# Kernel optimization log

Hardware: AMD Instinct MI355X
Metric: run time of the kernel (lower is better)

The kernel has to match this reference:

```python
import jax, jax.numpy as jnp
import numpy as np

INIT_SCALE = 5

def _steps(n_full):
    half = [i + 1 for i in range(0, int(n_full) + 1, 2)]
    return list(reversed(half[1:])) + half

STEP_H = np.array(_steps(192 / INIT_SCALE), dtype=np.float32)  # len 39
STEP_W = np.array(_steps(256 / INIT_SCALE), dtype=np.float32)  # len 51
MASK_H, MASK_W = len(STEP_H), len(STEP_W)


def _prelu(x, a):
    return jnp.maximum(x, 0.0) + a * jnp.minimum(x, 0.0)


def _reduce(x, w, b, a):
    # Conv2dBlock(64,4,1,1,norm='none',activation='prelu'): activation BEFORE 1x1 conv (per source)
    return jnp.einsum('nchw,oc->nohw', _prelu(x, a), w) + b[None, :, None, None]


def _crop_coords(cx, cy, H, W):
    # replicates floor(center - mask/2) / floor(center + mask/2) + border clamping
    top = cy - (MASK_H + 1) // 2
    bottom = cy + MASK_H // 2
    left = cx - (MASK_W + 1) // 2
    right = cx + MASK_W // 2
    dy1 = jnp.maximum(-top, 0)
    dy2 = jnp.maximum(bottom - H, 0)
    dx1 = jnp.maximum(-left, 0)
    dx2 = jnp.maximum(right - W, 0)
    new_top = top + dy1
    new_left = left + dx1
    new_h = jnp.maximum(bottom - dy2 - new_top, 0)
    new_w = jnp.maximum(right - dx2 - new_left, 0)
    return new_top, new_left, new_h, new_w, dy1, dx1


def _gimg(img, rows, cols):  # img (C,H,W) -> (C,len(rows),len(cols))
    return img[:, rows[:, None], cols[None, :]]


def _gmask(m, rows, cols):  # m (MASK_H,MASK_W)
    return m[rows[:, None], cols[None, :]]


def _forward(location, fea_c, fea_p, scale_param, H, W, c_landmark, p_landmark, w1, b1, a1, w2, b2, a2):
    N = fea_c.shape[0]
    ratio = H // fea_c.shape[2]
    fea_cn = _reduce(jnp.repeat(jnp.repeat(fea_c, ratio, 2), ratio, 3), w1, b1, a1)
    fea_pn = _reduce(jnp.repeat(jnp.repeat(fea_p, ratio, 2), ratio, 3), w2, b2, a2)
    C = fea_cn.shape[1]

    init_h = W / INIT_SCALE  # note: swapped vs H/W, exactly as in the original forward
    init_w = H / INIT_SCALE
    sig = jax.nn.sigmoid
    adj_cw, adj_ch = scale_param[:, :, 0, 0], scale_param[:, :, 0, 1]
    adj_pw, adj_ph = scale_param[:, :, 1, 0], scale_param[:, :, 1, 1]
    step_h = jnp.asarray(STEP_H)
    step_w = jnp.asarray(STEP_W)

    def box_mask(adj_h, adj_w):
        h = (init_h * sig(adj_h))[..., None]  # (N,32,1)
        w = (init_w * sig(adj_w))[..., None]
        return sig((h - step_h) * 2)[..., :, None] * sig((w - step_w) * 2)[..., None, :]

    src_mask = box_mask(adj_ch, adj_cw)  # (N,32,39,51)
    tar_mask = box_mask(adj_ph, adj_pw)

    r_ar = jnp.arange(MASK_H, dtype=jnp.int32)
    c_ar = jnp.arange(MASK_W, dtype=jnp.int32)
    c_cx, c_cy = c_landmark[:, :, 0], c_landmark[:, :, 1]
    p_cx, p_cy = p_landmark[:, :, 0], p_landmark[:, :, 1]
    use_lm = ~(((c_cx == 0) & (c_cy == 0)) | ((p_cx == 0) & (p_cy == 0)))  # (N,32)

    def make_patch(fea, lm_mask, cx, cy):
        top, left, nh, nw, dy1, dx1 = _crop_coords(cx, cy, H, W)
        rows = jnp.clip(top[..., None] + r_ar, 0, H - 1)        # (N,32,39)
        cols = jnp.clip(left[..., None] + c_ar, 0, W - 1)       # (N,32,51)
        mrows = jnp.clip(dy1[..., None] + r_ar, 0, MASK_H - 1)
        mcols = jnp.clip(dx1[..., None] + c_ar, 0, MASK_W - 1)
        valid = (use_lm[..., None, None]
                 & (r_ar[None, None, :, None] < nh[..., None, None])
                 & (c_ar[None, None, None, :] < nw[..., None, None]))  # (N,32,39,51)
        g = jax.vmap(lambda f, R, Cc: jax.vmap(_gimg, in_axes=(None, 0, 0))(f, R, Cc))(fea, rows, cols)  # (N,32,C,39,51)
        m = jax.vmap(jax.vmap(_gmask))(lm_mask, mrows, mcols)  # (N,32,39,51)
        patch = jnp.where(valid[:, :, None], g * m[:, :, None], 0.0)
        return patch, rows, cols, valid

    cloth, rows_c, cols_c, valid_c = make_patch(fea_cn, src_mask, c_cx, c_cy)
    person, rows_p, cols_p, valid_p = make_patch(fea_pn, tar_mask, p_cx, p_cy)

    loc5 = location.reshape(N, 32, 2, H, W)
    loc_g = jax.vmap(jax.vmap(_gimg))(loc5, rows_c, cols_c)  # (N,32,2,39,51)
    loc_patch = jnp.where(valid_c[:, :, None], loc_g, -1.0)  # -1 fill as in source

    L = MASK_H * MASK_W
    P = person.reshape(N, 32, C, L)
    K = cloth.reshape(N, 32, C, L)
    V = loc_patch.reshape(N, 32, 2, L)
    scores = jnp.einsum('nicp,nicq->nipq', P, K)  # (N,32,L,L) query=person px, key=cloth px
    corr = jax.nn.softmax(scores, axis=-1)
    flow_patch = jnp.einsum('nipq,nidq->nidp', corr, V).reshape(N, 32, 2, MASK_H, MASK_W)

    # scatter person-crop regions back into full-res outputs (invalid -> dump row/col H,W)
    rr = jnp.where(valid_p, jnp.broadcast_to(rows_p[:, :, :, None], valid_p.shape), H)
    cc = jnp.where(valid_p, jnp.broadcast_to(cols_p[:, :, None, :], valid_p.shape), W)
    bb = jnp.arange(N)[:, None, None, None]
    ii = jnp.arange(32)[None, :, None, None]
    flow_pad = jnp.full((N, 32, H + 1, W + 1, 2), -1.0, dtype=flow_patch.dtype)
    flow_pad = flow_pad.at[bb, ii, rr, cc].set(flow_patch.transpose(0, 1, 3, 4, 2))
    landmark_flow = flow_pad[:, :, :H, :W, :].transpose(0, 1, 4, 2, 3).reshape(N, 64, H, W)
    mask = jnp.zeros((N, 32, H + 1, W + 1), dtype=flow_patch.dtype).at[bb, ii, rr, cc].set(1.0)[:, :, :H, :W]
    return landmark_flow, mask


def setup_inputs() -> dict:
    key = jax.random.key(0)
    ks = jax.random.split(key, 8)
    N, H, W = 1, 192, 256
    fh, fw = H // 4, W // 4
    return {
        'location': jax.random.normal(ks[0], (N, 64, H, W), jnp.float32),
        'fea_c': jax.random.normal(ks[1], (N, 64, fh, fw), jnp.float32),
        'fea_p': jax.random.normal(ks[2], (N, 64, fh, fw), jnp.float32),
        'scale_param': jax.random.normal(ks[3], (N, 32, 2, 2), jnp.float32),
        'H': H,
        'W': W,
        'c_landmark': jax.random.randint(ks[4], (N, 32, 2), 0, 180, jnp.int32),
        'p_landmark': jax.random.randint(ks[5], (N, 32, 2), 0, 180, jnp.int32),
        'w1': jax.random.normal(ks[6], (4, 64), jnp.float32) * 0.05,
        'b1': jnp.zeros((4,), jnp.float32),
        'a1': jnp.array(0.25, jnp.float32),
        'w2': jax.random.normal(ks[7], (4, 64), jnp.float32) * 0.05,
        'b2': jnp.zeros((4,), jnp.float32),
        'a2': jnp.array(0.25, jnp.float32),
    }


def reference(location, fea_c, fea_p, scale_param, H, W, c_landmark, p_landmark, w1, b1, a1, w2, b2, a2):
    return _forward(location, fea_c, fea_p, scale_param, H, W, c_landmark, p_landmark, w1, b1, a1, w2, b2, a2)
```

## Files before the change

kernel.cpp:

```cpp
#include <hip/hip_runtime.h>

constexpr int kH = 192, kW = 256, kHW = kH * kW;
constexpr int kFH = 48, kFW = 64, kFHW = kFH * kFW;
constexpr int kMH = 39, kMW = 51;
constexpr int kL = kMH * kMW;
constexpr int kLP = 2048;
constexpr int kHeads = 32;
constexpr float kInitH = 256.0f / 5.0f;
constexpr float kInitW = 192.0f / 5.0f;
constexpr float kL2E = 1.44269504088896340736f;
constexpr float kBias = -16.0f;
constexpr float kPadCorr = 59.0f / 65536.0f;

typedef float v2f __attribute__((ext_vector_type(2)));
__device__ __forceinline__ v2f pkfma(v2f a, v2f b, v2f c) {
  return __builtin_elementwise_fma(a, b, c);
}

__device__ __forceinline__ float fast_exp2(float x) {
#if __has_builtin(__builtin_amdgcn_exp2f)
  return __builtin_amdgcn_exp2f(x);
#else
  float r;
  asm("v_exp_f32 %0, %1\n\ts_nop 1" : "=v"(r) : "v"(x));
  return r;
#endif
}

struct HeadParams {
  int use;
  int ntop_c, nleft_c, nh_c, nw_c, dy1_c, dx1_c;
  int ntop_p, nleft_p, nh_p, nw_p, dy1_p, dx1_p;
  float h_c, w_c, h_p, w_p;
};

__device__ __forceinline__ float sigf(float x) { return 1.0f / (1.0f + __expf(-x)); }
__device__ __forceinline__ float stepH(int j) { return (float)(2 * abs(j - 19) + 1); }
__device__ __forceinline__ float stepW(int j) { return (float)(2 * abs(j - 25) + 1); }

__device__ void headParams(int i, const int* clm, const int* plm, const float* sp, HeadParams& h) {
  int ccx = clm[2 * i], ccy = clm[2 * i + 1];
  int pcx = plm[2 * i], pcy = plm[2 * i + 1];
  h.use = !(((ccx == 0) && (ccy == 0)) || ((pcx == 0) && (pcy == 0)));
  {
    int top = ccy - (kMH + 1) / 2, bottom = ccy + kMH / 2;
    int left = ccx - (kMW + 1) / 2, right = ccx + kMW / 2;
    int dy1 = max(-top, 0), dy2 = max(bottom - kH, 0);
    int dx1 = max(-left, 0), dx2 = max(right - kW, 0);
    h.ntop_c = top + dy1; h.nleft_c = left + dx1; h.dy1_c = dy1; h.dx1_c = dx1;
    h.nh_c = max(kMH - dy1 - dy2, 0); h.nw_c = max(kMW - dx1 - dx2, 0);
  }
  {
    int top = pcy - (kMH + 1) / 2, bottom = pcy + kMH / 2;
    int left = pcx - (kMW + 1) / 2, right = pcx + kMW / 2;
    int dy1 = max(-top, 0), dy2 = max(bottom - kH, 0);
    int dx1 = max(-left, 0), dx2 = max(right - kW, 0);
    h.ntop_p = top + dy1; h.nleft_p = left + dx1; h.dy1_p = dy1; h.dx1_p = dx1;
    h.nh_p = max(kMH - dy1 - dy2, 0); h.nw_p = max(kMW - dx1 - dx2, 0);
  }
  float adj_cw = sp[4 * i + 0], adj_ch = sp[4 * i + 1];
  float adj_pw = sp[4 * i + 2], adj_ph = sp[4 * i + 3];
  h.h_c = kInitH * sigf(adj_ch);
  h.w_c = kInitW * sigf(adj_cw);
  h.h_p = kInitH * sigf(adj_ph);
  h.w_p = kInitW * sigf(adj_pw);
}

__global__ void k_init(float4* __restrict__ out, int n4, int nflow4) {
  int i = blockIdx.x * 256 + threadIdx.x;
  if (i < n4) {
    float v = (i < nflow4) ? -1.0f : 0.0f;
    out[i] = make_float4(v, v, v, v);
  }
}

__global__ void k_reduce(const float* __restrict__ fc, const float* __restrict__ fp,
                         const float* __restrict__ w1, const float* __restrict__ b1, const float* __restrict__ a1,
                         const float* __restrict__ w2, const float* __restrict__ b2, const float* __restrict__ a2,
                         float* __restrict__ fr) {
  int gid = blockIdx.x * 256 + threadIdx.x;
  if (gid >= 2 * kFHW) return;
  int which = gid / kFHW;
  int pix = gid - which * kFHW;
  const float* f = which ? fp : fc;
  const float* w = which ? w2 : w1;
  const float* b = which ? b2 : b1;
  float a = which ? a2[0] : a1[0];
  float acc0 = 0.f, acc1 = 0.f, acc2 = 0.f, acc3 = 0.f;
  for (int c = 0; c < 64; ++c) {
    float x = f[c * kFHW + pix];
    float pr = fmaxf(x, 0.f) + a * fminf(x, 0.f);
    acc0 = fmaf(pr, w[c], acc0);
    acc1 = fmaf(pr, w[64 + c], acc1);
    acc2 = fmaf(pr, w[128 + c], acc2);
    acc3 = fmaf(pr, w[192 + c], acc3);
  }
  float* o = fr + which * 4 * kFHW;
  o[pix]            = acc0 + b[0];
  o[kFHW + pix]     = acc1 + b[1];
  o[2 * kFHW + pix] = acc2 + b[2];
  o[3 * kFHW + pix] = acc3 + b[3];
}

__global__ void k_patch(const float* __restrict__ fr, const float* __restrict__ loc,
                        const float* __restrict__ sp, const int* __restrict__ clm, const int* __restrict__ plm,
                        float* __restrict__ Kpl, float* __restrict__ Vpl, float4* __restrict__ Pall) {
  int i = blockIdx.y;
  int q = blockIdx.x * 256 + threadIdx.x;
  HeadParams hp; headParams(i, clm, plm, sp, hp);
  int qr = q / kMW, qc = q - qr * kMW;
  constexpr int PS = kHeads * kLP;
  int o = i * kLP + q;
  {
    bool val = (q < kL) && hp.use && (qr < hp.nh_c) && (qc < hp.nw_c);
    int row = min(hp.ntop_c + qr, kH - 1);
    int col = min(hp.nleft_c + qc, kW - 1);
    int mr = min(hp.dy1_c + qr, kMH - 1);
    int mc = min(hp.dx1_c + qc, kMW - 1);
    float mv = sigf((hp.h_c - stepH(mr)) * 2.f) * sigf((hp.w_c - stepW(mc)) * 2.f);
    int fpix = (row >> 2) * kFW + (col >> 2);
    float kx = 0.f, ky = 0.f, kz = 0.f, kw = 0.f, vx = -1.f, vy = -1.f;
    if (val) {
      kx = fr[fpix] * mv;
      ky = fr[kFHW + fpix] * mv;
      kz = fr[2 * kFHW + fpix] * mv;
      kw = fr[3 * kFHW + fpix] * mv;
      vx = loc[(2 * i) * kHW + row * kW + col];
      vy = loc[(2 * i + 1) * kHW + row * kW + col];
    }
    Kpl[o] = kx; Kpl[PS + o] = ky; Kpl[2 * PS + o] = kz; Kpl[3 * PS + o] = kw;
    Vpl[o] = vx; Vpl[PS + o] = vy;
  }
  if (q < kL) {
    bool val = hp.use && (qr < hp.nh_p) && (qc < hp.nw_p);
    int row = min(hp.ntop_p + qr, kH - 1);
    int col = min(hp.nleft_p + qc, kW - 1);
    int mr = min(hp.dy1_p + qr, kMH - 1);
    int mc = min(hp.dx1_p + qc, kMW - 1);
    float mv = sigf((hp.h_p - stepH(mr)) * 2.f) * sigf((hp.w_p - stepW(mc)) * 2.f) * kL2E;
    int fpix = (row >> 2) * kFW + (col >> 2);
    float4 pv = make_float4(0.f, 0.f, 0.f, 0.f);
    if (val) {
      const float* frp = fr + 4 * kFHW;
      pv.x = frp[fpix] * mv;
      pv.y = frp[kFHW + fpix] * mv;
      pv.z = frp[2 * kFHW + fpix] * mv;
      pv.w = frp[3 * kFHW + fpix] * mv;
    }
    Pall[i * kL + q] = pv;
  }
}

template<int QLEN>
__global__ void __launch_bounds__(256) k_attn_t(const float* __restrict__ Kpl, const float* __restrict__ Vpl,
                                                const float4* __restrict__ Pall,
                                                float* __restrict__ pD, float* __restrict__ pX,
                                                float* __restrict__ pY) {
  constexpr int PS = kHeads * kLP;
  int i = blockIdx.z;
  int qsi = blockIdx.y;
  int p = blockIdx.x * 249 + threadIdx.x;
  int pe = min(p, kL - 1);
  const int base = i * kLP + qsi * QLEN;
  const float* kx = Kpl + base;
  const float* ky = Kpl + PS + base;
  const float* kz = Kpl + 2 * PS + base;
  const float* kw = Kpl + 3 * PS + base;
  const float* vx = Vpl + base;
  const float* vy = Vpl + PS + base;
  float4 P = Pall[i * kL + pe];
  v2f PX = {P.x, P.x}, PY = {P.y, P.y}, PZ = {P.z, P.z}, PW = {P.w, P.w};
  const v2f B = {kBias, kBias};
  v2f dA = {0.f, 0.f}, dB = {0.f, 0.f};
  v2f xA = {0.f, 0.f}, xB = {0.f, 0.f};
  v2f yA = {0.f, 0.f}, yB = {0.f, 0.f};
#pragma unroll 8
  for (int t = 0; t < QLEN; t += 4) {
    v2f sA = pkfma(PW, *(const v2f*)(kw + t), B);
    sA = pkfma(PZ, *(const v2f*)(kz + t), sA);
    sA = pkfma(PY, *(const v2f*)(ky + t), sA);
    sA = pkfma(PX, *(const v2f*)(kx + t), sA);
    v2f sB = pkfma(PW, *(const v2f*)(kw + t + 2), B);
    sB = pkfma(PZ, *(const v2f*)(kz + t + 2), sB);
    sB = pkfma(PY, *(const v2f*)(ky + t + 2), sB);
    sB = pkfma(PX, *(const v2f*)(kx + t + 2), sB);
    v2f eA = {fast_exp2(sA.x), fast_exp2(sA.y)};
    v2f eB = {fast_exp2(sB.x), fast_exp2(sB.y)};
    dA += eA;
    xA = pkfma(eA, *(const v2f*)(vx + t), xA);
    yA = pkfma(eA, *(const v2f*)(vy + t), yA);
    dB += eB;
    xB = pkfma(eB, *(const v2f*)(vx + t + 2), xB);
    yB = pkfma(eB, *(const v2f*)(vy + t + 2), yB);
  }
  int o = (i * gridDim.y + qsi) * kLP + pe;
  pD[o] = dA.x + dA.y + dB.x + dB.y;
  pX[o] = xA.x + xA.y + xB.x + xB.y;
  pY[o] = yA.x + yA.y + yB.x + yB.y;
}

__global__ void k_merge(const float* __restrict__ pD, const float* __restrict__ pX, const float* __restrict__ pY,
                        int QS,
                        const float* __restrict__ sp, const int* __restrict__ clm, const int* __restrict__ plm,
                        float* __restrict__ out) {
  int i = blockIdx.y;
  int p = blockIdx.x * 256 + threadIdx.x;
  if (p >= kL) return;
  HeadParams hp; headParams(i, clm, plm, sp, hp);

  int pr = p / kMW, pc = p - pr * kMW;
  bool val = hp.use && (pr < hp.nh_p) && (pc < hp.nw_p);
  if (!val) return;

  float den = -kPadCorr, n0 = kPadCorr, n1 = kPadCorr;
  for (int k = 0; k < QS; ++k) {
    int o = (i * QS + k) * kLP + p;
    den += pD[o]; n0 += pX[o]; n1 += pY[o];
  }
  float inv = 1.0f / den;
  float f0 = n0 * inv, f1 = n1 * inv;

  int R = hp.ntop_p + pr;
  int C = hp.nleft_p + pc;
  out[(2 * i) * kHW + R * kW + C] = f0;
  out[(2 * i + 1) * kHW + R * kW + C] = f1;
  out[64 * kHW + i * kHW + R * kW + C] = 1.0f;
}

extern "C" void kernel_launch(void* const* d_in, const int* in_sizes, int n_in,
                              void* d_out, int out_size, void* d_ws, size_t ws_size,
                              hipStream_t stream) {
  (void)in_sizes; (void)n_in;
  const float* loc = (const float*)d_in[0];
  const float* fc  = (const float*)d_in[1];
  const float* fp  = (const float*)d_in[2];
  const float* sp  = (const float*)d_in[3];
  const int* clm   = (const int*)d_in[6];
  const int* plm   = (const int*)d_in[7];
  const float* w1  = (const float*)d_in[8];
  const float* b1  = (const float*)d_in[9];
  const float* a1  = (const float*)d_in[10];
  const float* w2  = (const float*)d_in[11];
  const float* b2  = (const float*)d_in[12];
  const float* a2  = (const float*)d_in[13];
  float* out = (float*)d_out;
  char* ws = (char*)d_ws;

  float*  fr   = (float*)(ws);
  float*  Kpl  = (float*)(ws + 98304);
  float*  Vpl  = (float*)(ws + 1146880);
  float4* Pall = (float4*)(ws + 1671168);
  size_t base = 2689536;
  size_t perQS = (size_t)3 * kHeads * kLP * 4;
  int QS = 1;
  if (ws_size >= base + 16 * perQS) QS = 16;
  else if (ws_size >= base + 8 * perQS) QS = 8;
  else if (ws_size >= base + 4 * perQS) QS = 4;
  else if (ws_size >= base + 2 * perQS) QS = 2;
  float* pD = (float*)(ws + base);
  float* pX = pD + (size_t)QS * kHeads * kLP;
  float* pY = pX + (size_t)QS * kHeads * kLP;

  int n4 = out_size / 4;
  int nflow4 = 64 * kHW / 4;
  k_init<<<(n4 + 255) / 256, 256, 0, stream>>>((float4*)out, n4, nflow4);
  k_reduce<<<(2 * kFHW + 255) / 256, 256, 0, stream>>>(fc, fp, w1, b1, a1, w2, b2, a2, fr);
  k_patch<<<dim3(kLP / 256, kHeads), 256, 0, stream>>>(fr, loc, sp, clm, plm, Kpl, Vpl, Pall);
  dim3 ag(8, QS, kHeads);
  switch (QS) {
    case 16: k_attn_t<128><<<ag, 256, 0, stream>>>(Kpl, Vpl, Pall, pD, pX, pY); break;
    case 8:  k_attn_t<256><<<ag, 256, 0, stream>>>(Kpl, Vpl, Pall, pD, pX, pY); break;
    case 4:  k_attn_t<512><<<ag, 256, 0, stream>>>(Kpl, Vpl, Pall, pD, pX, pY); break;
    case 2:  k_attn_t<1024><<<ag, 256, 0, stream>>>(Kpl, Vpl, Pall, pD, pX, pY); break;
    default: k_attn_t<2048><<<ag, 256, 0, stream>>>(Kpl, Vpl, Pall, pD, pX, pY); break;
  }
  k_merge<<<dim3((kL + 255) / 256, kHeads), 256, 0, stream>>>(pD, pX, pY, QS, sp, clm, plm, out);
}
```

Baseline: 59.83 us.

## Fuse output init into full-image merge and precompute per-head parameters

Removes the separate k_init kernel by having the merge kernel cover every output pixel, writing either the computed flow and mask or the default fill values. Per-head crop parameters are computed once by an extra block in the reduce kernel, stored in workspace and read by patch and merge instead of being recomputed per thread. This drops one launch and avoids a double write of the output, at the cost of merge launching far more threads (full image per head) and a heavier extra block in the pre kernel.

```diff
diff --git a/kernel.cpp b/kernel.cpp
--- a/kernel.cpp
+++ b/kernel.cpp
@@ -66,20 +66,26 @@
   h.w_p = kInitW * sigf(adj_pw);
 }
 
-__global__ void k_init(float4* __restrict__ out, int n4, int nflow4) {
-  int i = blockIdx.x * 256 + threadIdx.x;
-  if (i < n4) {
-    float v = (i < nflow4) ? -1.0f : 0.0f;
-    out[i] = make_float4(v, v, v, v);
-  }
-}
-
-__global__ void k_reduce(const float* __restrict__ fc, const float* __restrict__ fp,
-                         const float* __restrict__ w1, const float* __restrict__ b1, const float* __restrict__ a1,
-                         const float* __restrict__ w2, const float* __restrict__ b2, const float* __restrict__ a2,
-                         float* __restrict__ fr) {
-  int gid = blockIdx.x * 256 + threadIdx.x;
-  if (gid >= 2 * kFHW) return;
+__global__ void k_pre(const float* __restrict__ fc, const float* __restrict__ fp,
+                      const float* __restrict__ w1, const float* __restrict__ b1, const float* __restrict__ a1,
+                      const float* __restrict__ w2, const float* __restrict__ b2, const float* __restrict__ a2,
+                      const float* __restrict__ sp, const int* __restrict__ clm, const int* __restrict__ plm,
+                      float* __restrict__ fr, int* __restrict__ hpws) {
+  int bx = blockIdx.x;
+  if (bx == 24) {
+    int i = threadIdx.x;
+    if (i < kHeads) {
+      HeadParams h; headParams(i, clm, plm, sp, h);
+      int* o = hpws + i * 20;
+      o[0] = h.use;
+      o[1] = h.ntop_c; o[2] = h.nleft_c; o[3] = h.nh_c; o[4] = h.nw_c; o[5] = h.dy1_c; o[6] = h.dx1_c;
+      o[7] = h.ntop_p; o[8] = h.nleft_p; o[9] = h.nh_p; o[10] = h.nw_p; o[11] = h.dy1_p; o[12] = h.dx1_p;
+      o[13] = __float_as_int(h.h_c); o[14] = __float_as_int(h.w_c);
+      o[15] = __float_as_int(h.h_p); o[16] = __float_as_int(h.w_p);
+    }
+    return;
+  }
+  int gid = bx * 256 + threadIdx.x;
   int which = gid / kFHW;
   int pix = gid - which * kFHW;
   const float* f = which ? fp : fc;
@@ -103,21 +109,26 @@
 }
 
 __global__ void k_patch(const float* __restrict__ fr, const float* __restrict__ loc,
-                        const float* __restrict__ sp, const int* __restrict__ clm, const int* __restrict__ plm,
+                        const int* __restrict__ hpws,
                         float* __restrict__ Kpl, float* __restrict__ Vpl, float4* __restrict__ Pall) {
   int i = blockIdx.y;
   int q = blockIdx.x * 256 + threadIdx.x;
-  HeadParams hp; headParams(i, clm, plm, sp, hp);
+  const int* hp = hpws + i * 20;
+  int use = hp[0];
+  int ntop_c = hp[1], nleft_c = hp[2], nh_c = hp[3], nw_c = hp[4], dy1_c = hp[5], dx1_c = hp[6];
+  int ntop_p = hp[7], nleft_p = hp[8], nh_p = hp[9], nw_p = hp[10], dy1_p = hp[11], dx1_p = hp[12];
+  float h_c = __int_as_float(hp[13]), w_c = __int_as_float(hp[14]);
+  float h_p = __int_as_float(hp[15]), w_p = __int_as_float(hp[16]);
   int qr = q / kMW, qc = q - qr * kMW;
   constexpr int PS = kHeads * kLP;
   int o = i * kLP + q;
   {
-    bool val = (q < kL) && hp.use && (qr < hp.nh_c) && (qc < hp.nw_c);
-    int row = min(hp.ntop_c + qr, kH - 1);
-    int col = min(hp.nleft_c + qc, kW - 1);
-    int mr = min(hp.dy1_c + qr, kMH - 1);
-    int mc = min(hp.dx1_c + qc, kMW - 1);
-    float mv = sigf((hp.h_c - stepH(mr)) * 2.f) * sigf((hp.w_c - stepW(mc)) * 2.f);
+    bool val = (q < kL) && use && (qr < nh_c) && (qc < nw_c);
+    int row = min(ntop_c + qr, kH - 1);
+    int col = min(nleft_c + qc, kW - 1);
+    int mr = min(dy1_c + qr, kMH - 1);
+    int mc = min(dx1_c + qc, kMW - 1);
+    float mv = sigf((h_c - stepH(mr)) * 2.f) * sigf((w_c - stepW(mc)) * 2.f);
     int fpix = (row >> 2) * kFW + (col >> 2);
     float kx = 0.f, ky = 0.f, kz = 0.f, kw = 0.f, vx = -1.f, vy = -1.f;
     if (val) {
@@ -132,12 +143,12 @@
     Vpl[o] = vx; Vpl[PS + o] = vy;
   }
   if (q < kL) {
-    bool val = hp.use && (qr < hp.nh_p) && (qc < hp.nw_p);
-    int row = min(hp.ntop_p + qr, kH - 1);
-    int col = min(hp.nleft_p + qc, kW - 1);
-    int mr = min(hp.dy1_p + qr, kMH - 1);
-    int mc = min(hp.dx1_p + qc, kMW - 1);
-    float mv = sigf((hp.h_p - stepH(mr)) * 2.f) * sigf((hp.w_p - stepW(mc)) * 2.f) * kL2E;
+    bool val = use && (qr < nh_p) && (qc < nw_p);
+    int row = min(ntop_p + qr, kH - 1);
+    int col = min(nleft_p + qc, kW - 1);
+    int mr = min(dy1_p + qr, kMH - 1);
+    int mc = min(dx1_p + qc, kMW - 1);
+    float mv = sigf((h_p - stepH(mr)) * 2.f) * sigf((w_p - stepW(mc)) * 2.f) * kL2E;
     int fpix = (row >> 2) * kFW + (col >> 2);
     float4 pv = make_float4(0.f, 0.f, 0.f, 0.f);
     if (val) {
@@ -199,38 +210,38 @@
   pY[o] = yA.x + yA.y + yB.x + yB.y;
 }
 
-__global__ void k_merge(const float* __restrict__ pD, const float* __restrict__ pX, const float* __restrict__ pY,
-                        int QS,
-                        const float* __restrict__ sp, const int* __restrict__ clm, const int* __restrict__ plm,
-                        float* __restrict__ out) {
+__global__ void k_merge_full(const float* __restrict__ pD, const float* __restrict__ pX,
+                             const float* __restrict__ pY, int QS,
+                             const int* __restrict__ hpws, float* __restrict__ out) {
   int i = blockIdx.y;
-  int p = blockIdx.x * 256 + threadIdx.x;
-  if (p >= kL) return;
-  HeadParams hp; headParams(i, clm, plm, sp, hp);
-
-  int pr = p / kMW, pc = p - pr * kMW;
-  bool val = hp.use && (pr < hp.nh_p) && (pc < hp.nw_p);
-  if (!val) return;
-
-  float den = -kPadCorr, n0 = kPadCorr, n1 = kPadCorr;
-  for (int k = 0; k < QS; ++k) {
-    int o = (i * QS + k) * kLP + p;
-    den += pD[o]; n0 += pX[o]; n1 += pY[o];
-  }
-  float inv = 1.0f / den;
-  float f0 = n0 * inv, f1 = n1 * inv;
-
-  int R = hp.ntop_p + pr;
-  int C = hp.nleft_p + pc;
-  out[(2 * i) * kHW + R * kW + C] = f0;
-  out[(2 * i + 1) * kHW + R * kW + C] = f1;
-  out[64 * kHW + i * kHW + R * kW + C] = 1.0f;
+  int pix = blockIdx.x * 256 + threadIdx.x;
+  const int* hp = hpws + i * 20;
+  int use = hp[0];
+  int ntop_p = hp[7], nleft_p = hp[8], nh_p = hp[9], nw_p = hp[10];
+  int r = pix >> 8;
+  int c = pix & 255;
+  int pr = r - ntop_p, pc = c - nleft_p;
+  bool val = use && ((unsigned)pr < (unsigned)nh_p) && ((unsigned)pc < (unsigned)nw_p);
+  float f0 = -1.f, f1 = -1.f, mk = 0.f;
+  if (val) {
+    int p = pr * kMW + pc;
+    float den = -kPadCorr, n0 = kPadCorr, n1 = kPadCorr;
+    for (int k = 0; k < QS; ++k) {
+      int o = (i * QS + k) * kLP + p;
+      den += pD[o]; n0 += pX[o]; n1 += pY[o];
+    }
+    float inv = 1.0f / den;
+    f0 = n0 * inv; f1 = n1 * inv; mk = 1.0f;
+  }
+  out[(2 * i) * kHW + pix]      = f0;
+  out[(2 * i + 1) * kHW + pix]  = f1;
+  out[64 * kHW + i * kHW + pix] = mk;
 }
 
 extern "C" void kernel_launch(void* const* d_in, const int* in_sizes, int n_in,
                               void* d_out, int out_size, void* d_ws, size_t ws_size,
                               hipStream_t stream) {
-  (void)in_sizes; (void)n_in;
+  (void)in_sizes; (void)n_in; (void)out_size;
   const float* loc = (const float*)d_in[0];
   const float* fc  = (const float*)d_in[1];
   const float* fp  = (const float*)d_in[2];
@@ -246,11 +257,12 @@
   float* out = (float*)d_out;
   char* ws = (char*)d_ws;
 
-  float*  fr   = (float*)(ws);
-  float*  Kpl  = (float*)(ws + 98304);
-  float*  Vpl  = (float*)(ws + 1146880);
-  float4* Pall = (float4*)(ws + 1671168);
-  size_t base = 2689536;
+  int*    hpws = (int*)(ws);
+  float*  fr   = (float*)(ws + 4096);
+  float*  Kpl  = (float*)(ws + 102400);
+  float*  Vpl  = (float*)(ws + 1150976);
+  float4* Pall = (float4*)(ws + 1675264);
+  size_t base = 2693632;
   size_t perQS = (size_t)3 * kHeads * kLP * 4;
   int QS = 1;
   if (ws_size >= base + 16 * perQS) QS = 16;
@@ -261,11 +273,8 @@
   float* pX = pD + (size_t)QS * kHeads * kLP;
   float* pY = pX + (size_t)QS * kHeads * kLP;
 
-  int n4 = out_size / 4;
-  int nflow4 = 64 * kHW / 4;
-  k_init<<<(n4 + 255) / 256, 256, 0, stream>>>((float4*)out, n4, nflow4);
-  k_reduce<<<(2 * kFHW + 255) / 256, 256, 0, stream>>>(fc, fp, w1, b1, a1, w2, b2, a2, fr);
-  k_patch<<<dim3(kLP / 256, kHeads), 256, 0, stream>>>(fr, loc, sp, clm, plm, Kpl, Vpl, Pall);
+  k_pre<<<25, 256, 0, stream>>>(fc, fp, w1, b1, a1, w2, b2, a2, sp, clm, plm, fr, hpws);
+  k_patch<<<dim3(kLP / 256, kHeads), 256, 0, stream>>>(fr, loc, hpws, Kpl, Vpl, Pall);
   dim3 ag(8, QS, kHeads);
   switch (QS) {
     case 16: k_attn_t<128><<<ag, 256, 0, stream>>>(Kpl, Vpl, Pall, pD, pX, pY); break;
@@ -274,5 +283,5 @@
     case 2:  k_attn_t<1024><<<ag, 256, 0, stream>>>(Kpl, Vpl, Pall, pD, pX, pY); break;
     default: k_attn_t<2048><<<ag, 256, 0, stream>>>(Kpl, Vpl, Pall, pD, pX, pY); break;
   }
-  k_merge<<<dim3((kL + 255) / 256, kHeads), 256, 0, stream>>>(pD, pX, pY, QS, sp, clm, plm, out);
-}
+  k_merge_full<<<dim3(kHW / 256, kHeads), 256, 0, stream>>>(pD, pX, pY, QS, hpws, out);
+}
```

After: 57.03 us. 1.05x faster.
